# Optimization experiments

Hardware: AMD Instinct MI355X
Metric: run time of the kernel (lower is better)

Reference implementation:

```python
import jax, jax.numpy as jnp
import numpy as np

D, NH, DH, DM = 1024, 16, 64, 4096
B, S = 2, 2048
EPS = 1e-5


def _layernorm(x, w, b):
    mu = jnp.mean(x, axis=-1, keepdims=True)
    var = jnp.mean((x - mu) ** 2, axis=-1, keepdims=True)
    return (x - mu) * jax.lax.rsqrt(var + EPS) * w + b


def setup_inputs() -> dict:
    key = jax.random.key(0)
    ks = jax.random.split(key, 8)
    scale = D ** (-0.5)
    x = jax.random.normal(ks[0], (B, S, D), dtype=jnp.float32)
    WQ = jax.random.normal(ks[1], (NH, D, DH), dtype=jnp.float32) * scale
    WK = jax.random.normal(ks[2], (NH, D, DH), dtype=jnp.float32) * scale
    WV = jax.random.normal(ks[3], (NH, D, DH), dtype=jnp.float32) * scale
    WO = jax.random.normal(ks[4], (NH, DH, D), dtype=jnp.float32) * scale
    # MLP: torch Linear default init ~ U(-1/sqrt(fan_in), 1/sqrt(fan_in)); stored as [in, out]
    W1 = jax.random.uniform(ks[5], (D, DM), dtype=jnp.float32, minval=-1.0, maxval=1.0) * D ** (-0.5)
    b1 = jnp.zeros((DM,), dtype=jnp.float32)
    W2 = jax.random.uniform(ks[6], (DM, D), dtype=jnp.float32, minval=-1.0, maxval=1.0) * DM ** (-0.5)
    b2 = jnp.zeros((D,), dtype=jnp.float32)
    ln1_w = jnp.ones((D,), dtype=jnp.float32)
    ln1_b = jnp.zeros((D,), dtype=jnp.float32)
    ln2_w = jnp.ones((D,), dtype=jnp.float32)
    ln2_b = jnp.zeros((D,), dtype=jnp.float32)
    return {"x": x, "WQ": WQ, "WK": WK, "WV": WV, "WO": WO,
            "W1": W1, "b1": b1, "W2": W2, "b2": b2,
            "ln1_w": ln1_w, "ln1_b": ln1_b, "ln2_w": ln2_w, "ln2_b": ln2_b}


def reference(x, WQ, WK, WV, WO, W1, b1, W2, b2, ln1_w, ln1_b, ln2_w, ln2_b):
    s = x.shape[1]
    dh = WQ.shape[-1]
    r = x
    h = _layernorm(x, ln1_w, ln1_b)
    # batched across all heads (original loops over h; math identical)
    Q = jnp.einsum('bsd,hde->bhse', h, WQ)
    K = jnp.einsum('bsd,hde->bhse', h, WK)
    V = jnp.einsum('bsd,hde->bhse', h, WV)
    scores = jnp.einsum('bhqe,bhke->bhqk', Q, K) / jnp.sqrt(jnp.float32(dh))
    causal = jnp.tril(jnp.ones((s, s), dtype=bool))  # True = keep
    scores = jnp.where(causal, scores, -jnp.inf)
    attn = jax.nn.softmax(scores, axis=-1)
    ctx = jnp.einsum('bhqk,bhke->bhqe', attn, V)
    ao = jnp.einsum('bhqe,hed->bqd', ctx, WO)  # sum over heads
    x = r + ao
    h2 = _layernorm(x, ln2_w, ln2_b)
    mlp = jax.nn.gelu(h2 @ W1 + b1, approximate=False) @ W2 + b2
    return x + mlp
```

## Files before the change

kernel.cpp:

```cpp
#include <hip/hip_runtime.h>
#include <hip/hip_bf16.h>
#include <cstdint>

#define D_MODEL 1024
#define NHEADS 16
#define DHEAD 64
#define DMLP 4096
#define BATCH 2
#define SEQ 2048
#define ROWS (BATCH*SEQ)
#define LN_EPS 1e-5f

typedef __attribute__((ext_vector_type(8))) short short8;
typedef __attribute__((ext_vector_type(4))) float f32x4;

typedef const __attribute__((address_space(1))) uint32_t* gas_ptr;
typedef __attribute__((address_space(3))) uint32_t* las_ptr;

__device__ __forceinline__ short f2bf(float f) {
  union { float f; uint32_t u; } v; v.f = f;
  uint32_t r = v.u + 0x7FFFu + ((v.u >> 16) & 1u);
  return (short)(r >> 16);
}
__device__ __forceinline__ float bf2f(short s) {
  union { uint32_t u; float f; } v; v.u = ((uint32_t)(uint16_t)s) << 16;
  return v.f;
}

__global__ void ln_kernel(const float* __restrict__ x, const float* __restrict__ w,
                          const float* __restrict__ b, short* __restrict__ out) {
  int row = blockIdx.x;
  int t = threadIdx.x;
  const float4 v = ((const float4*)(x + (size_t)row * D_MODEL))[t];
  float s = v.x + v.y + v.z + v.w;
  float s2 = v.x*v.x + v.y*v.y + v.z*v.z + v.w*v.w;
#pragma unroll
  for (int k = 1; k < 64; k <<= 1) { s += __shfl_xor(s, k); s2 += __shfl_xor(s2, k); }
  __shared__ float red[8];
  int wv = t >> 6;
  if ((t & 63) == 0) { red[wv] = s; red[wv + 4] = s2; }
  __syncthreads();
  s = red[0] + red[1] + red[2] + red[3];
  s2 = red[4] + red[5] + red[6] + red[7];
  float mu = s * (1.0f / D_MODEL);
  float var = s2 * (1.0f / D_MODEL) - mu * mu;
  float rstd = rsqrtf(var + LN_EPS);
  const float4 wv4 = ((const float4*)w)[t];
  const float4 bv4 = ((const float4*)b)[t];
  short4 o4;
  o4.x = f2bf((v.x - mu) * rstd * wv4.x + bv4.x);
  o4.y = f2bf((v.y - mu) * rstd * wv4.y + bv4.y);
  o4.z = f2bf((v.z - mu) * rstd * wv4.z + bv4.z);
  o4.w = f2bf((v.w - mu) * rstd * wv4.w + bv4.w);
  *(short4*)(out + (size_t)row * D_MODEL + t * 4) = o4;
}

__global__ void repack_qkv(const float* __restrict__ WQ, const float* __restrict__ WK,
                           const float* __restrict__ WV, short* __restrict__ out) {
  int id = blockIdx.x * 256 + threadIdx.x;
  int d = id & 1023;
  int n = id >> 10;
  int proj = n >> 10;
  int he = n & 1023;
  int h = he >> 6, e = he & 63;
  const float* W = (proj == 0) ? WQ : ((proj == 1) ? WK : WV);
  out[id] = f2bf(W[h * (D_MODEL * DHEAD) + d * DHEAD + e]);
}

__global__ void transpose_cvt(const float* __restrict__ src, short* __restrict__ dst,
                              int R, int Cbits) {
  int id = blockIdx.x * 256 + threadIdx.x;
  int r = id >> Cbits;
  int c = id & ((1 << Cbits) - 1);
  dst[(size_t)c * R + r] = f2bf(src[id]);
}

template<int EPI>
__global__ __launch_bounds__(256) void gemm_bt(const short* __restrict__ A, const short* __restrict__ BT,
                        const float* __restrict__ bias, const float* __restrict__ resid,
                        float* __restrict__ outf, short* __restrict__ outb,
                        int M, int N, int K) {
  __shared__ alignas(16) short As[128 * 32];
  __shared__ alignas(16) short Bs[128 * 32];
  const int t = threadIdx.x;
  const int l = t & 63;
  const int w = t >> 6;
  const int row0 = blockIdx.y * 128, col0 = blockIdx.x * 128;

  f32x4 acc[4][4] = {};

  const int srow = w * 16 + (l >> 2);
  const int schunk = (l & 3) * 8;
  const short* Abase = A + (size_t)(row0 + srow) * K + schunk;
  const short* Bbase = BT + (size_t)(col0 + srow) * K + schunk;
  char* AsB = (char*)As;
  char* BsB = (char*)Bs;
  const int ldsoff = w * 1024 + l * 16;

  const int wr = (w >> 1) * 64, wc = (w & 1) * 64;
  const int lk = (l >> 4) * 8;
  const int lr16 = l & 15;

  for (int k0 = 0; k0 < K; k0 += 32) {
    __builtin_amdgcn_global_load_lds((gas_ptr)(Abase + k0),          (las_ptr)(AsB + ldsoff),        16, 0, 0);
    __builtin_amdgcn_global_load_lds((gas_ptr)(Abase + 64 * K + k0), (las_ptr)(AsB + 4096 + ldsoff), 16, 0, 0);
    __builtin_amdgcn_global_load_lds((gas_ptr)(Bbase + k0),          (las_ptr)(BsB + ldsoff),        16, 0, 0);
    __builtin_amdgcn_global_load_lds((gas_ptr)(Bbase + 64 * K + k0), (las_ptr)(BsB + 4096 + ldsoff), 16, 0, 0);
    __syncthreads();

    short8 a[4], bfr[4];
#pragma unroll
    for (int m = 0; m < 4; m++) a[m]   = *(const short8*)&As[(wr + m * 16 + lr16) * 32 + lk];
#pragma unroll
    for (int n = 0; n < 4; n++) bfr[n] = *(const short8*)&Bs[(wc + n * 16 + lr16) * 32 + lk];
#pragma unroll
    for (int m = 0; m < 4; m++)
#pragma unroll
      for (int n = 0; n < 4; n++)
        acc[m][n] = __builtin_amdgcn_mfma_f32_16x16x32_bf16(a[m], bfr[n], acc[m][n], 0, 0, 0);
    __syncthreads();
  }

#pragma unroll
  for (int m = 0; m < 4; m++) {
#pragma unroll
    for (int n = 0; n < 4; n++) {
#pragma unroll
      for (int j = 0; j < 4; j++) {
        int R_ = row0 + wr + m * 16 + (l >> 4) * 4 + j;
        int C_ = col0 + wc + n * 16 + lr16;
        float v = acc[m][n][j];
        size_t o = (size_t)R_ * N + C_;
        if (EPI == 0) {
          outb[o] = f2bf(v);
        } else if (EPI == 1) {
          outf[o] = v + resid[o];
        } else if (EPI == 2) {
          float xx = v + bias[C_];
          outb[o] = f2bf(0.5f * xx * (1.0f + erff(xx * 0.70710678118f)));
        } else {
          outf[o] = v + bias[C_] + resid[o];
        }
      }
    }
  }
}

__device__ __forceinline__ void attn_step(
    int kt_, int qt, int bufP,
    const short* __restrict__ base, const short* __restrict__ vbase,
    short8& vWA, short8& vWB,
    short8& vLA, short8& vLB,
    const short8 qf[2],
    char* KsB, char* VtB, char* PlB,
    f32x4 acc[4], float mrun[4], float lrun[4], float* alphaOut,
    int w, int l, int q0, int vr, int vd0)
{
  const int l15 = l & 15, l4 = l >> 4;
  const int bufQ = bufP ^ 1;
  if (kt_ < qt) {
#pragma unroll
    for (int i = 0; i < 8; i++) {
      int d = vd0 + i;
      int cs = (vr >> 2) ^ ((d >> 3) & 7);
      uint32_t val = (uint32_t)(uint16_t)vWA[i] | ((uint32_t)(uint16_t)vWB[i] << 16);
      *(uint32_t*)(VtB + bufQ * 9216 + d * 144 + cs * 16 + (vr & 3) * 4) = val;
    }
#pragma unroll
    for (int i = 0; i < 2; i++) {
      int g = (w * 2 + i) * 64 + l;
      int key = g >> 3, ck = g & 7;
      const short* src = base + (size_t)((kt_ + 1) * 64 + key) * 3072 + 1024 + ((ck ^ (key & 7)) * 8);
      __builtin_amdgcn_global_load_lds((gas_ptr)src, (las_ptr)(KsB + bufQ * 8192 + g * 16), 16, 0, 0);
    }
  }
  if (kt_ + 2 <= qt) {
    vLA = *(const short8*)(vbase + (size_t)((kt_ + 2) * 64 + 2 * vr) * 3072);
    vLB = *(const short8*)(vbase + (size_t)((kt_ + 2) * 64 + 2 * vr + 1) * 3072);
  }

  f32x4 sc[4];
#pragma unroll
  for (int cb = 0; cb < 4; cb++) {
    f32x4 s = {};
    int key = cb * 16 + l15;
#pragma unroll
    for (int c = 0; c < 2; c++) {
      int ck = (c * 4 + l4) ^ (key & 7);
      short8 kf = *(const short8*)(KsB + bufP * 8192 + key * 128 + ck * 16);
      s = __builtin_amdgcn_mfma_f32_16x16x32_bf16(qf[c], kf, s, 0, 0, 0);
    }
    sc[cb] = s;
  }

  const bool lastt = (kt_ == qt);
  float alpha[4];
#pragma unroll
  for (int jj = 0; jj < 4; jj++) {
    int qg = q0 + l4 * 4 + jj;
    float s0 = sc[0][jj] * 0.125f;
    float s1 = sc[1][jj] * 0.125f;
    float s2 = sc[2][jj] * 0.125f;
    float s3 = sc[3][jj] * 0.125f;
    if (lastt) {
      int kg = kt_ * 64 + l15;
      if (kg      > qg) s0 = -1e30f;
      if (kg + 16 > qg) s1 = -1e30f;
      if (kg + 32 > qg) s2 = -1e30f;
      if (kg + 48 > qg) s3 = -1e30f;
    }
    float rm = fmaxf(fmaxf(s0, s1), fmaxf(s2, s3));
    rm = fmaxf(rm, __shfl_xor(rm, 1));
    rm = fmaxf(rm, __shfl_xor(rm, 2));
    rm = fmaxf(rm, __shfl_xor(rm, 4));
    rm = fmaxf(rm, __shfl_xor(rm, 8));
    float nm = fmaxf(mrun[jj], rm);
    float al = __expf(mrun[jj] - nm);
    mrun[jj] = nm;
    float p0 = __expf(s0 - nm), p1 = __expf(s1 - nm);
    float p2 = __expf(s2 - nm), p3 = __expf(s3 - nm);
    float ps = p0 + p1 + p2 + p3;
    ps += __shfl_xor(ps, 1);
    ps += __shfl_xor(ps, 2);
    ps += __shfl_xor(ps, 4);
    ps += __shfl_xor(ps, 8);
    lrun[jj] = lrun[jj] * al + ps;
    alpha[jj] = al;
    short* pr = (short*)(PlB + (l4 * 4 + jj) * 144);
    pr[l15]      = f2bf(p0);
    pr[16 + l15] = f2bf(p1);
    pr[32 + l15] = f2bf(p2);
    pr[48 + l15] = f2bf(p3);
  }
#pragma unroll
  for (int db = 0; db < 4; db++) {
    f32x4 a = acc[db];
    a[0] *= alpha[0]; a[1] *= alpha[1]; a[2] *= alpha[2]; a[3] *= alpha[3];
    acc[db] = a;
  }
#pragma unroll
  for (int kc = 0; kc < 2; kc++) {
    short8 pf = *(const short8*)(PlB + l15 * 144 + kc * 64 + l4 * 16);
#pragma unroll
    for (int db = 0; db < 4; db++) {
      int d = db * 16 + l15;
      int cs = (kc * 4 + l4) ^ ((d >> 3) & 7);
      short8 vf = *(const short8*)(VtB + bufP * 9216 + d * 144 + cs * 16);
      acc[db] = __builtin_amdgcn_mfma_f32_16x16x32_bf16(pf, vf, acc[db], 0, 0, 0);
    }
  }
  (void)alphaOut;
}

__global__ __launch_bounds__(256) void attn_mfma(const short* __restrict__ qkv, short* __restrict__ ctx) {
  __shared__ alignas(16) short Ks[2 * 64 * 64];
  __shared__ alignas(16) short Vt[2 * 64 * 72];
  __shared__ alignas(16) short Pl[4][16 * 72];
  const int t = threadIdx.x;
  const int l = t & 63;
  const int w = t >> 6;
  const int l15 = l & 15, l4 = l >> 4;
  const int bh = blockIdx.x;
  const int b = bh >> 4, h = bh & 15;
  const int qt = (gridDim.y - 1) - blockIdx.y;
  const int q0 = qt * 64 + w * 16;

  const short* base = qkv + (size_t)b * SEQ * 3072 + h * 64;

  short8 qf[2];
#pragma unroll
  for (int c = 0; c < 2; c++)
    qf[c] = *(const short8*)(base + (size_t)(q0 + l15) * 3072 + c * 32 + l4 * 8);

  const int vr = t >> 3;
  const int vd0 = (t & 7) * 8;
  const short* vbase = base + 2048 + vd0;

  char* KsB = (char*)Ks;
  char* VtB = (char*)Vt;
  char* PlB = (char*)&Pl[w][0];

  short8 va0, vb0, va1, vb1;
  va0 = *(const short8*)(vbase + (size_t)(2 * vr) * 3072);
  vb0 = *(const short8*)(vbase + (size_t)(2 * vr + 1) * 3072);
  if (qt >= 1) {
    va1 = *(const short8*)(vbase + (size_t)(64 + 2 * vr) * 3072);
    vb1 = *(const short8*)(vbase + (size_t)(64 + 2 * vr + 1) * 3072);
  }
#pragma unroll
  for (int i = 0; i < 8; i++) {
    int d = vd0 + i;
    int cs = (vr >> 2) ^ ((d >> 3) & 7);
    uint32_t val = (uint32_t)(uint16_t)va0[i] | ((uint32_t)(uint16_t)vb0[i] << 16);
    *(uint32_t*)(VtB + d * 144 + cs * 16 + (vr & 3) * 4) = val;
  }
#pragma unroll
  for (int i = 0; i < 2; i++) {
    int g = (w * 2 + i) * 64 + l;
    int key = g >> 3, ck = g & 7;
    const short* src = base + (size_t)key * 3072 + 1024 + ((ck ^ (key & 7)) * 8);
    __builtin_amdgcn_global_load_lds((gas_ptr)src, (las_ptr)(KsB + g * 16), 16, 0, 0);
  }
  __syncthreads();

  f32x4 acc[4] = {};
  float mrun[4] = {-1e30f, -1e30f, -1e30f, -1e30f};
  float lrun[4] = {0.f, 0.f, 0.f, 0.f};

  int kt = 0;
  while (true) {
    attn_step(kt, qt, 0, base, vbase, va1, vb1, va0, vb0, qf,
              KsB, VtB, PlB, acc, mrun, lrun, nullptr, w, l, q0, vr, vd0);
    __syncthreads();
    if (++kt > qt) break;
    attn_step(kt, qt, 1, base, vbase, va0, vb0, va1, vb1, qf,
              KsB, VtB, PlB, acc, mrun, lrun, nullptr, w, l, q0, vr, vd0);
    __syncthreads();
    if (++kt > qt) break;
  }

  float inv[4];
#pragma unroll
  for (int jj = 0; jj < 4; jj++) inv[jj] = 1.0f / lrun[jj];
  short* obase = ctx + (size_t)(b * SEQ + q0) * D_MODEL + h * 64;
#pragma unroll
  for (int db = 0; db < 4; db++)
#pragma unroll
    for (int jj = 0; jj < 4; jj++)
      obase[(size_t)(l4 * 4 + jj) * D_MODEL + db * 16 + l15] = f2bf(acc[db][jj] * inv[jj]);
}

extern "C" void kernel_launch(void* const* d_in, const int* in_sizes, int n_in,
                              void* d_out, int out_size, void* d_ws, size_t ws_size,
                              hipStream_t stream) {
  (void)in_sizes; (void)n_in; (void)out_size; (void)ws_size;
  const float* x    = (const float*)d_in[0];
  const float* WQ   = (const float*)d_in[1];
  const float* WK   = (const float*)d_in[2];
  const float* WV   = (const float*)d_in[3];
  const float* WO   = (const float*)d_in[4];
  const float* W1   = (const float*)d_in[5];
  const float* b1   = (const float*)d_in[6];
  const float* W2   = (const float*)d_in[7];
  const float* b2   = (const float*)d_in[8];
  const float* ln1w = (const float*)d_in[9];
  const float* ln1b = (const float*)d_in[10];
  const float* ln2w = (const float*)d_in[11];
  const float* ln2b = (const float*)d_in[12];
  float* out = (float*)d_out;

  char* p = (char*)d_ws;
  short* h1    = (short*)p; p += (size_t)ROWS * D_MODEL * 2;
  short* ctx   = (short*)p; p += (size_t)ROWS * D_MODEL * 2;
  short* h2    = (short*)p; p += (size_t)ROWS * D_MODEL * 2;
  short* m1    = (short*)p; p += (size_t)ROWS * DMLP * 2;
  short* wqkvT = (short*)p; p += (size_t)3 * D_MODEL * D_MODEL * 2;
  short* woT   = (short*)p; p += (size_t)D_MODEL * D_MODEL * 2;
  short* w1T   = (short*)p; p += (size_t)D_MODEL * DMLP * 2;
  short* w2T   = (short*)p; p += (size_t)D_MODEL * DMLP * 2;
  short* qkv   = (short*)p; p += (size_t)ROWS * 3 * D_MODEL * 2;

  repack_qkv<<<3 * D_MODEL * D_MODEL / 256, 256, 0, stream>>>(WQ, WK, WV, wqkvT);
  transpose_cvt<<<D_MODEL * D_MODEL / 256, 256, 0, stream>>>(WO, woT, D_MODEL, 10);
  transpose_cvt<<<D_MODEL * DMLP / 256, 256, 0, stream>>>(W1, w1T, D_MODEL, 12);
  transpose_cvt<<<D_MODEL * DMLP / 256, 256, 0, stream>>>(W2, w2T, DMLP, 10);

  ln_kernel<<<ROWS, 256, 0, stream>>>(x, ln1w, ln1b, h1);
  gemm_bt<0><<<dim3(3 * D_MODEL / 128, ROWS / 128), 256, 0, stream>>>(
      h1, wqkvT, nullptr, nullptr, nullptr, qkv, ROWS, 3 * D_MODEL, D_MODEL);
  attn_mfma<<<dim3(BATCH * NHEADS, SEQ / 64), 256, 0, stream>>>(qkv, ctx);
  gemm_bt<1><<<dim3(D_MODEL / 128, ROWS / 128), 256, 0, stream>>>(
      ctx, woT, nullptr, x, out, nullptr, ROWS, D_MODEL, D_MODEL);
  ln_kernel<<<ROWS, 256, 0, stream>>>(out, ln2w, ln2b, h2);
  gemm_bt<2><<<dim3(DMLP / 128, ROWS / 128), 256, 0, stream>>>(
      h2, w1T, b1, nullptr, nullptr, m1, ROWS, DMLP, D_MODEL);
  gemm_bt<3><<<dim3(D_MODEL / 128, ROWS / 128), 256, 0, stream>>>(
      m1, w2T, b2, out, out, nullptr, ROWS, D_MODEL, DMLP);
}
```

Measured before the change: 362.1 us.

## Double-buffer GEMM LDS tiles with XOR swizzle and tile weight transposes

The GEMM now double-buffers its A/B LDS tiles, prefetching the next K slice with global_load_lds while the current one feeds MFMA, which removes one barrier per iteration. An XOR swizzle on the 16-byte chunk index is meant to cut LDS bank conflicts on fragment reads. The scattered per-element weight repack and transpose kernels are replaced by a shared-memory tiled transpose with coalesced float4 reads and short4 writes. Doubling the LDS footprint may lower occupancy.

```diff
diff --git a/kernel.cpp b/kernel.cpp
--- a/kernel.cpp
+++ b/kernel.cpp
@@ -55,24 +55,34 @@
   *(short4*)(out + (size_t)row * D_MODEL + t * 4) = o4;
 }
 
-__global__ void repack_qkv(const float* __restrict__ WQ, const float* __restrict__ WK,
-                           const float* __restrict__ WV, short* __restrict__ out) {
-  int id = blockIdx.x * 256 + threadIdx.x;
-  int d = id & 1023;
-  int n = id >> 10;
-  int proj = n >> 10;
-  int he = n & 1023;
-  int h = he >> 6, e = he & 63;
-  const float* W = (proj == 0) ? WQ : ((proj == 1) ? WK : WV);
-  out[id] = f2bf(W[h * (D_MODEL * DHEAD) + d * DHEAD + e]);
-}
-
-__global__ void transpose_cvt(const float* __restrict__ src, short* __restrict__ dst,
-                              int R, int Cbits) {
-  int id = blockIdx.x * 256 + threadIdx.x;
-  int r = id >> Cbits;
-  int c = id & ((1 << Cbits) - 1);
-  dst[(size_t)c * R + r] = f2bf(src[id]);
+__global__ __launch_bounds__(256) void transpose_tile(const float* __restrict__ src, short* __restrict__ dst,
+                                                      int R, int C, int srcMatStride) {
+  __shared__ float tile[64][65];
+  const int m = blockIdx.z;
+  const int r0 = blockIdx.y * 64, c0 = blockIdx.x * 64;
+  const int tx = threadIdx.x & 15, ty = threadIdx.x >> 4;
+  const float* s = src + (size_t)m * srcMatStride + (size_t)r0 * C + c0;
+#pragma unroll
+  for (int i = 0; i < 4; i++) {
+    float4 v = *(const float4*)(s + (size_t)(ty + i * 16) * C + tx * 4);
+    tile[ty + i * 16][tx * 4 + 0] = v.x;
+    tile[ty + i * 16][tx * 4 + 1] = v.y;
+    tile[ty + i * 16][tx * 4 + 2] = v.z;
+    tile[ty + i * 16][tx * 4 + 3] = v.w;
+  }
+  __syncthreads();
+  short* d = dst + (size_t)m * C * R + (size_t)c0 * R + r0;
+#pragma unroll
+  for (int p = 0; p < 4; p++) {
+    int c = ty + p * 16;
+    int r4 = tx * 4;
+    short4 o;
+    o.x = f2bf(tile[r4 + 0][c]);
+    o.y = f2bf(tile[r4 + 1][c]);
+    o.z = f2bf(tile[r4 + 2][c]);
+    o.w = f2bf(tile[r4 + 3][c]);
+    *(short4*)(d + (size_t)c * R + r4) = o;
+  }
 }
 
 template<int EPI>
@@ -80,8 +90,8 @@
                         const float* __restrict__ bias, const float* __restrict__ resid,
                         float* __restrict__ outf, short* __restrict__ outb,
                         int M, int N, int K) {
-  __shared__ alignas(16) short As[128 * 32];
-  __shared__ alignas(16) short Bs[128 * 32];
+  __shared__ alignas(16) short As[2][128 * 32];
+  __shared__ alignas(16) short Bs[2][128 * 32];
   const int t = threadIdx.x;
   const int l = t & 63;
   const int w = t >> 6;
@@ -90,29 +100,41 @@
   f32x4 acc[4][4] = {};
 
   const int srow = w * 16 + (l >> 2);
-  const int schunk = (l & 3) * 8;
-  const short* Abase = A + (size_t)(row0 + srow) * K + schunk;
-  const short* Bbase = BT + (size_t)(col0 + srow) * K + schunk;
+  const int cs8 = ((l & 3) ^ (srow & 3)) * 8;
+  const short* Abase = A + (size_t)(row0 + srow) * K + cs8;
+  const short* Bbase = BT + (size_t)(col0 + srow) * K + cs8;
   char* AsB = (char*)As;
   char* BsB = (char*)Bs;
   const int ldsoff = w * 1024 + l * 16;
 
   const int wr = (w >> 1) * 64, wc = (w & 1) * 64;
-  const int lk = (l >> 4) * 8;
-  const int lr16 = l & 15;
-
-  for (int k0 = 0; k0 < K; k0 += 32) {
-    __builtin_amdgcn_global_load_lds((gas_ptr)(Abase + k0),          (las_ptr)(AsB + ldsoff),        16, 0, 0);
-    __builtin_amdgcn_global_load_lds((gas_ptr)(Abase + 64 * K + k0), (las_ptr)(AsB + 4096 + ldsoff), 16, 0, 0);
-    __builtin_amdgcn_global_load_lds((gas_ptr)(Bbase + k0),          (las_ptr)(BsB + ldsoff),        16, 0, 0);
-    __builtin_amdgcn_global_load_lds((gas_ptr)(Bbase + 64 * K + k0), (las_ptr)(BsB + 4096 + ldsoff), 16, 0, 0);
-    __syncthreads();
-
+  const int l15 = l & 15, l4 = l >> 4;
+  const int rchunk = (l4 ^ (l15 & 3)) * 8;
+
+  __builtin_amdgcn_global_load_lds((gas_ptr)(Abase),          (las_ptr)(AsB + ldsoff),        16, 0, 0);
+  __builtin_amdgcn_global_load_lds((gas_ptr)(Abase + 64 * K), (las_ptr)(AsB + 4096 + ldsoff), 16, 0, 0);
+  __builtin_amdgcn_global_load_lds((gas_ptr)(Bbase),          (las_ptr)(BsB + ldsoff),        16, 0, 0);
+  __builtin_amdgcn_global_load_lds((gas_ptr)(Bbase + 64 * K), (las_ptr)(BsB + 4096 + ldsoff), 16, 0, 0);
+  __syncthreads();
+
+  const int nk = K >> 5;
+  for (int ti = 0; ti < nk; ti++) {
+    const int cur = ti & 1;
+    if (ti + 1 < nk) {
+      const int nb = (cur ^ 1) * 8192;
+      const int k0 = (ti + 1) << 5;
+      __builtin_amdgcn_global_load_lds((gas_ptr)(Abase + k0),          (las_ptr)(AsB + nb + ldsoff),        16, 0, 0);
+      __builtin_amdgcn_global_load_lds((gas_ptr)(Abase + 64 * K + k0), (las_ptr)(AsB + nb + 4096 + ldsoff), 16, 0, 0);
+      __builtin_amdgcn_global_load_lds((gas_ptr)(Bbase + k0),          (las_ptr)(BsB + nb + ldsoff),        16, 0, 0);
+      __builtin_amdgcn_global_load_lds((gas_ptr)(Bbase + 64 * K + k0), (las_ptr)(BsB + nb + 4096 + ldsoff), 16, 0, 0);
+    }
+    const short* Ab = &As[cur][0];
+    const short* Bb = &Bs[cur][0];
     short8 a[4], bfr[4];
 #pragma unroll
-    for (int m = 0; m < 4; m++) a[m]   = *(const short8*)&As[(wr + m * 16 + lr16) * 32 + lk];
-#pragma unroll
-    for (int n = 0; n < 4; n++) bfr[n] = *(const short8*)&Bs[(wc + n * 16 + lr16) * 32 + lk];
+    for (int m = 0; m < 4; m++) a[m]   = *(const short8*)&Ab[(wr + m * 16 + l15) * 32 + rchunk];
+#pragma unroll
+    for (int n = 0; n < 4; n++) bfr[n] = *(const short8*)&Bb[(wc + n * 16 + l15) * 32 + rchunk];
 #pragma unroll
     for (int m = 0; m < 4; m++)
 #pragma unroll
@@ -127,8 +149,8 @@
     for (int n = 0; n < 4; n++) {
 #pragma unroll
       for (int j = 0; j < 4; j++) {
-        int R_ = row0 + wr + m * 16 + (l >> 4) * 4 + j;
-        int C_ = col0 + wc + n * 16 + lr16;
+        int R_ = row0 + wr + m * 16 + l4 * 4 + j;
+        int C_ = col0 + wc + n * 16 + l15;
         float v = acc[m][n][j];
         size_t o = (size_t)R_ * N + C_;
         if (EPI == 0) {
@@ -153,7 +175,7 @@
     short8& vLA, short8& vLB,
     const short8 qf[2],
     char* KsB, char* VtB, char* PlB,
-    f32x4 acc[4], float mrun[4], float lrun[4], float* alphaOut,
+    f32x4 acc[4], float mrun[4], float lrun[4],
     int w, int l, int q0, int vr, int vd0)
 {
   const int l15 = l & 15, l4 = l >> 4;
@@ -249,7 +271,6 @@
       acc[db] = __builtin_amdgcn_mfma_f32_16x16x32_bf16(pf, vf, acc[db], 0, 0, 0);
     }
   }
-  (void)alphaOut;
 }
 
 __global__ __launch_bounds__(256) void attn_mfma(const short* __restrict__ qkv, short* __restrict__ ctx) {
@@ -310,11 +331,11 @@
   int kt = 0;
   while (true) {
     attn_step(kt, qt, 0, base, vbase, va1, vb1, va0, vb0, qf,
-              KsB, VtB, PlB, acc, mrun, lrun, nullptr, w, l, q0, vr, vd0);
+              KsB, VtB, PlB, acc, mrun, lrun, w, l, q0, vr, vd0);
     __syncthreads();
     if (++kt > qt) break;
     attn_step(kt, qt, 1, base, vbase, va0, vb0, va1, vb1, qf,
-              KsB, VtB, PlB, acc, mrun, lrun, nullptr, w, l, q0, vr, vd0);
+              KsB, VtB, PlB, acc, mrun, lrun, w, l, q0, vr, vd0);
     __syncthreads();
     if (++kt > qt) break;
   }
@@ -360,10 +381,12 @@
   short* w2T   = (short*)p; p += (size_t)D_MODEL * DMLP * 2;
   short* qkv   = (short*)p; p += (size_t)ROWS * 3 * D_MODEL * 2;
 
-  repack_qkv<<<3 * D_MODEL * D_MODEL / 256, 256, 0, stream>>>(WQ, WK, WV, wqkvT);
-  transpose_cvt<<<D_MODEL * D_MODEL / 256, 256, 0, stream>>>(WO, woT, D_MODEL, 10);
-  transpose_cvt<<<D_MODEL * DMLP / 256, 256, 0, stream>>>(W1, w1T, D_MODEL, 12);
-  transpose_cvt<<<D_MODEL * DMLP / 256, 256, 0, stream>>>(W2, w2T, DMLP, 10);
+  transpose_tile<<<dim3(1, 16, 16), 256, 0, stream>>>(WQ, wqkvT,                  1024, 64, D_MODEL * DHEAD);
+  transpose_tile<<<dim3(1, 16, 16), 256, 0, stream>>>(WK, wqkvT + 1024 * 1024,    1024, 64, D_MODEL * DHEAD);
+  transpose_tile<<<dim3(1, 16, 16), 256, 0, stream>>>(WV, wqkvT + 2 * 1024 * 1024, 1024, 64, D_MODEL * DHEAD);
+  transpose_tile<<<dim3(16, 16, 1), 256, 0, stream>>>(WO, woT, 1024, 1024, 0);
+  transpose_tile<<<dim3(64, 16, 1), 256, 0, stream>>>(W1, w1T, 1024, 4096, 0);
+  transpose_tile<<<dim3(16, 64, 1), 256, 0, stream>>>(W2, w2T, 4096, 1024, 0);
 
   ln_kernel<<<ROWS, 256, 0, stream>>>(x, ln1w, ln1b, h1);
   gemm_bt<0><<<dim3(3 * D_MODEL / 128, ROWS / 128), 256, 0, stream>>>(
```

New measurement: 308.1 us. 14.9% less time.
